# Kernel tuning notes

Measured on AMD Instinct MI355X. Metric: run time of the kernel, lower is better.

## Reference

```python
import jax, jax.numpy as jnp
import numpy as np


def _ln(x, s, b, eps=1e-5):
    m = x.mean(-1, keepdims=True)
    v = ((x - m) ** 2).mean(-1, keepdims=True)
    return (x - m) / jnp.sqrt(v + eps) * s + b


def setup_inputs() -> dict:
    key = jax.random.key(0)
    ks = jax.random.split(key, 12)
    B, T, H, W, C, heads = 4, 4, 16, 16, 128, 8
    N = H * W
    Ntot = T * N
    hid = int(C * 2.66)  # 340

    def rn(k, shape, scale=0.02):
        return jax.random.normal(k, shape, jnp.float32) * scale

    return dict(
        x=jax.random.normal(ks[0], (B, Ntot, C), jnp.float32),
        bias=jax.random.normal(ks[1], (B, Ntot, Ntot), jnp.float32),
        ln1_s=jnp.ones(C), ln1_b=jnp.zeros(C),
        qkv_w=rn(ks[2], (3 * C, C)), qkv_b=jnp.zeros(3 * C),
        proj_w=rn(ks[3], (C, C)), proj_b=jnp.zeros(C),
        bw1=rn(ks[4], (16, 1), 0.5), bb1=jnp.zeros(16),
        bw2=rn(ks[5], (heads, 16), 0.5), bb2=jnp.zeros(heads),
        ln2_s=jnp.ones(C), ln2_b=jnp.zeros(C),
        pin_w=rn(ks[6], (2 * hid, C, 1, 1)), pin_b=jnp.zeros(2 * hid),
        dw_w=rn(ks[7], (2 * hid, 1, 3, 3)), dw_b=jnp.zeros(2 * hid),
        pout_w=rn(ks[8], (C, hid, 1, 1)), pout_b=jnp.zeros(C),
        gamma1=1e-4 * jnp.ones(C), gamma2=1e-4 * jnp.ones(C),
        T=T, H=H, W=W,
    )


def reference(x, bias, ln1_s, ln1_b, qkv_w, qkv_b, proj_w, proj_b,
              bw1, bb1, bw2, bb2, ln2_s, ln2_b,
              pin_w, pin_b, dw_w, dw_b, pout_w, pout_b,
              gamma1, gamma2, T, H, W):
    B, Ntot, C = x.shape
    heads = bw2.shape[0]
    d = C // heads

    # --- attention branch ---
    xn = _ln(x, ln1_s, ln1_b)
    qkv = (xn @ qkv_w.T + qkv_b).reshape(B, Ntot, 3, heads, d).transpose(2, 0, 3, 1, 4)
    q, k, v = qkv[0], qkv[1], qkv[2]  # (B, heads, Ntot, d)
    attn = jnp.einsum('bhnd,bhmd->bhnm', q, k) * (d ** -0.5)
    # NonLinearLieBias: Linear(1,16) -> ReLU -> Linear(16,heads), per (i,j) pair
    lb = jax.nn.relu(bias[..., None] * bw1[:, 0] + bb1) @ bw2.T + bb2  # (B,N,N,heads)
    attn = attn + lb.transpose(0, 3, 1, 2)
    attn = jax.nn.softmax(attn, axis=-1)
    out = jnp.einsum('bhnm,bhmd->bhnd', attn, v).transpose(0, 2, 1, 3).reshape(B, Ntot, C)
    out = out @ proj_w.T + proj_b
    x = x + gamma1 * out

    # --- GDFN branch ---
    N = H * W
    xn2 = _ln(x, ln2_s, ln2_b)
    y = xn2.reshape(B, T, N, C).transpose(0, 1, 3, 2).reshape(B * T, C, H, W)
    dn = ('NCHW', 'OIHW', 'NCHW')
    y = jax.lax.conv_general_dilated(y, pin_w, (1, 1), 'VALID', dimension_numbers=dn) + pin_b[None, :, None, None]
    y = jax.lax.conv_general_dilated(y, dw_w, (1, 1), ((1, 1), (1, 1)), dimension_numbers=dn,
                                     feature_group_count=y.shape[1]) + dw_b[None, :, None, None]
    hid = y.shape[1] // 2
    y = jax.nn.gelu(y[:, :hid], approximate=False) * y[:, hid:]
    y = jax.lax.conv_general_dilated(y, pout_w, (1, 1), 'VALID', dimension_numbers=dn) + pout_b[None, :, None, None]
    y = y.reshape(B, T, C, N).transpose(0, 1, 3, 2).reshape(B, T * N, C)
    x = x + gamma2 * y
    return (x, attn)
```

## Files before the change

kernel.cpp:

```cpp
#include <hip/hip_runtime.h>
#include <hip/hip_bf16.h>
#include <math.h>

#define BB 4
#define NT 1024
#define NSP 256
#define C 128
#define HEADS 8
#define HID 340
#define HID2 680
#define EPS 1e-5f

#define WS_Q    0
#define WS_KT   524288
#define WS_VT   1048576
#define WS_AO   1572864
#define WS_X1   2097152
#define WS_XN2  2621440
#define WS_PIN  3145728
#define WS_GLU  5931008
#define WS_MISC 7323648

typedef __bf16 bf16x8 __attribute__((ext_vector_type(8)));
typedef float f32x4 __attribute__((ext_vector_type(4)));

__global__ void k0_prep(const float* __restrict__ bw1, const float* __restrict__ bb1,
                        const float* __restrict__ bw2, float* __restrict__ misc) {
    int t = threadIdx.x;
    if (t < HEADS) {
        float P = 0.f, Nn = 0.f;
        for (int k = 0; k < 16; ++k) {
            float w1 = bw1[k];
            float w2 = bw2[t * 16 + k];
            if (w1 > 0.f) P += w2 * w1; else Nn += w2 * w1;
        }
        misc[t] = P;
        misc[8 + t] = Nn;
    }
    if (t == 0) {
        int f = 1;
        for (int k = 0; k < 16; ++k) if (bb1[k] != 0.f) f = 0;
        misc[16] = (float)f;
    }
}

__global__ __launch_bounds__(256) void k1_ln_qkv(
    const float* __restrict__ x, const float* __restrict__ s1, const float* __restrict__ b1,
    const float* __restrict__ qkv_w, const float* __restrict__ qkv_b, float* __restrict__ ws) {
    __shared__ float sxn[8][C];
    __shared__ float part[4][2];
    int tid = threadIdx.x;
    int g = tid >> 7, c = tid & 127;
    int wv = tid >> 6, lane = tid & 63;
    int tb = blockIdx.x * 8;

    for (int pass = 0; pass < 4; ++pass) {
        int tok = pass * 2 + g;
        float v = x[(size_t)(tb + tok) * C + c];
        float s = v, sq = v * v;
        #pragma unroll
        for (int off = 32; off; off >>= 1) { s += __shfl_xor(s, off); sq += __shfl_xor(sq, off); }
        if (lane == 0) { part[wv][0] = s; part[wv][1] = sq; }
        __syncthreads();
        float tot = part[g * 2][0] + part[g * 2 + 1][0];
        float tot2 = part[g * 2][1] + part[g * 2 + 1][1];
        float m = tot * (1.0f / C);
        float var = tot2 * (1.0f / C) - m * m;
        float inv = rsqrtf(var + EPS);
        sxn[tok][c] = (v - m) * inv * s1[c] + b1[c];
        __syncthreads();
    }

    float* qw = ws + WS_Q;
    float* ktw = ws + WS_KT;
    float* vtw = ws + WS_VT;
    for (int oo = tid; oo < 384; oo += 256) {
        const float4* wr = (const float4*)(qkv_w + (size_t)oo * C);
        float bbv = qkv_b[oo];
        float acc[8];
        #pragma unroll
        for (int t = 0; t < 8; ++t) acc[t] = bbv;
        #pragma unroll 4
        for (int ic4 = 0; ic4 < 32; ++ic4) {
            float4 w4 = wr[ic4];
            #pragma unroll
            for (int t = 0; t < 8; ++t) {
                acc[t] += w4.x * sxn[t][ic4 * 4 + 0] + w4.y * sxn[t][ic4 * 4 + 1]
                        + w4.z * sxn[t][ic4 * 4 + 2] + w4.w * sxn[t][ic4 * 4 + 3];
            }
        }
        int m3 = oo >> 7, h = (oo >> 4) & 7, dd = oo & 15;
        for (int t = 0; t < 8; ++t) {
            int tok = tb + t;
            int b = tok >> 10, i = tok & 1023;
            if (m3 == 0)      qw[(size_t)tok * C + h * 16 + dd] = acc[t] * 0.25f;
            else if (m3 == 1) ktw[(((size_t)b * 8 + h) * 16 + dd) * NT + i] = acc[t];
            else              vtw[(((size_t)b * 8 + h) * 16 + dd) * NT + i] = acc[t];
        }
    }
}

__global__ __launch_bounds__(256, 4) void k2a_sm(
    const float* __restrict__ bias, const float* __restrict__ bb2v,
    const float* __restrict__ bw1v, const float* __restrict__ bb1v, const float* __restrict__ bw2v,
    const float* __restrict__ ws, float* __restrict__ attn_out) {
    int tid = threadIdx.x;
    int wv = tid >> 6, lane = tid & 63;
    int o = blockIdx.x;
    int blk = (o & 7) * 256 + (o >> 3);
    int b = blk >> 9;
    int quad = (blk >> 1) & 255;
    int hh = blk & 1;
    int i0 = quad << 2;
    int h = hh * 4 + wv;

    const float* misc = ws + WS_MISC;
    float Ph = misc[h], Nh = misc[8 + h], c2 = bb2v[h];
    bool fast = (misc[16] != 0.0f);

    float lg[4][16];
    #pragma unroll
    for (int r = 0; r < 4; ++r) {
        const float* brow = bias + ((size_t)(b * NT + i0 + r)) * NT;
        #pragma unroll
        for (int k = 0; k < 4; ++k) {
            float4 b4 = *(const float4*)(brow + k * 256 + lane * 4);
            float bv[4] = {b4.x, b4.y, b4.z, b4.w};
            #pragma unroll
            for (int cc = 0; cc < 4; ++cc) {
                float bvv = bv[cc];
                float lb;
                if (fast) {
                    lb = bvv * (bvv > 0.f ? Ph : Nh) + c2;
                } else {
                    lb = c2;
                    for (int kk = 0; kk < 16; ++kk) {
                        float t = bvv * bw1v[kk] + bb1v[kk];
                        if (t > 0.f) lb += bw2v[h * 16 + kk] * t;
                    }
                }
                lg[r][k * 4 + cc] = lb;
            }
        }
    }

    const float* ktb = ws + WS_KT + ((size_t)(b * 8 + h) * 16) * NT;
    const float* qb = ws + WS_Q + ((size_t)(b * NT + i0)) * C + h * 16;
    #pragma unroll
    for (int dg = 0; dg < 4; ++dg) {
        float4 q0 = *(const float4*)(qb + 0 * C + dg * 4);
        float4 q1 = *(const float4*)(qb + 1 * C + dg * 4);
        float4 q2 = *(const float4*)(qb + 2 * C + dg * 4);
        float4 q3 = *(const float4*)(qb + 3 * C + dg * 4);
        float qa0[4] = {q0.x, q0.y, q0.z, q0.w};
        float qa1[4] = {q1.x, q1.y, q1.z, q1.w};
        float qa2[4] = {q2.x, q2.y, q2.z, q2.w};
        float qa3[4] = {q3.x, q3.y, q3.z, q3.w};
        #pragma unroll
        for (int dd = 0; dd < 4; ++dd) {
            const float4* kr = (const float4*)(ktb + (size_t)(dg * 4 + dd) * NT);
            #pragma unroll
            for (int k = 0; k < 4; ++k) {
                float4 kv = kr[k * 64 + lane];
                lg[0][k*4+0] += qa0[dd]*kv.x; lg[0][k*4+1] += qa0[dd]*kv.y;
                lg[0][k*4+2] += qa0[dd]*kv.z; lg[0][k*4+3] += qa0[dd]*kv.w;
                lg[1][k*4+0] += qa1[dd]*kv.x; lg[1][k*4+1] += qa1[dd]*kv.y;
                lg[1][k*4+2] += qa1[dd]*kv.z; lg[1][k*4+3] += qa1[dd]*kv.w;
                lg[2][k*4+0] += qa2[dd]*kv.x; lg[2][k*4+1] += qa2[dd]*kv.y;
                lg[2][k*4+2] += qa2[dd]*kv.z; lg[2][k*4+3] += qa2[dd]*kv.w;
                lg[3][k*4+0] += qa3[dd]*kv.x; lg[3][k*4+1] += qa3[dd]*kv.y;
                lg[3][k*4+2] += qa3[dd]*kv.z; lg[3][k*4+3] += qa3[dd]*kv.w;
            }
        }
    }

    #pragma unroll
    for (int r = 0; r < 4; ++r) {
        float mx = lg[r][0];
        #pragma unroll
        for (int k = 1; k < 16; ++k) mx = fmaxf(mx, lg[r][k]);
        #pragma unroll
        for (int off = 32; off; off >>= 1) mx = fmaxf(mx, __shfl_xor(mx, off));
        float s = 0.f;
        #pragma unroll
        for (int k = 0; k < 16; ++k) { lg[r][k] = __expf(lg[r][k] - mx); s += lg[r][k]; }
        #pragma unroll
        for (int off = 32; off; off >>= 1) s += __shfl_xor(s, off);
        float inv = 1.0f / s;
        float* gbase = attn_out + ((size_t)(b * 8 + h) * NT + i0 + r) * NT;
        #pragma unroll
        for (int k = 0; k < 4; ++k) {
            float4 ov;
            ov.x = lg[r][k * 4 + 0] * inv; ov.y = lg[r][k * 4 + 1] * inv;
            ov.z = lg[r][k * 4 + 2] * inv; ov.w = lg[r][k * 4 + 3] * inv;
            *(float4*)(gbase + k * 256 + lane * 4) = ov;
        }
    }
}

__global__ __launch_bounds__(256) void k2b_pv(const float* __restrict__ attn,
                                              const float* __restrict__ ws_ro,
                                              float* __restrict__ ws_out) {
    __shared__ __bf16 sVT[16][1032];
    int tid = threadIdx.x;
    int blk = blockIdx.x;
    int bh = blk >> 4;
    int i0 = (blk & 15) * 64;
    const float* vt = ws_ro + WS_VT + (size_t)bh * 16 * NT;

    #pragma unroll
    for (int s = 0; s < 16; ++s) {
        int f4 = tid + 256 * s;
        int dd = f4 >> 8, jq = f4 & 255;
        float4 v4 = *(const float4*)(vt + ((size_t)dd << 10) + jq * 4);
        sVT[dd][jq * 4 + 0] = (__bf16)v4.x;
        sVT[dd][jq * 4 + 1] = (__bf16)v4.y;
        sVT[dd][jq * 4 + 2] = (__bf16)v4.z;
        sVT[dd][jq * 4 + 3] = (__bf16)v4.w;
    }
    __syncthreads();

    int wv = tid >> 6, lane = tid & 63;
    int row = lane & 15, kg = lane >> 4;
    const float* pbase = attn + ((size_t)bh * NT + i0 + wv * 16 + row) * NT;
    f32x4 acc = {0.f, 0.f, 0.f, 0.f};
    #pragma unroll 4
    for (int kt = 0; kt < 32; ++kt) {
        int k0 = kt * 32 + kg * 8;
        float4 a0 = *(const float4*)(pbase + k0);
        float4 a1 = *(const float4*)(pbase + k0 + 4);
        bf16x8 af;
        af[0] = (__bf16)a0.x; af[1] = (__bf16)a0.y; af[2] = (__bf16)a0.z; af[3] = (__bf16)a0.w;
        af[4] = (__bf16)a1.x; af[5] = (__bf16)a1.y; af[6] = (__bf16)a1.z; af[7] = (__bf16)a1.w;
        bf16x8 bfv = *(const bf16x8*)&sVT[row][k0];
        acc = __builtin_amdgcn_mfma_f32_16x16x32_bf16(af, bfv, acc, 0, 0, 0);
    }
    int b = bh >> 3, h = bh & 7;
    float* ao = ws_out + WS_AO;
    #pragma unroll
    for (int q = 0; q < 4; ++q) {
        int irow = i0 + wv * 16 + kg * 4 + q;
        ao[((size_t)(b * NT + irow)) * C + h * 16 + row] = acc[q];
    }
}

__global__ __launch_bounds__(256) void k3_proj(
    const float* __restrict__ x, const float* __restrict__ proj_w, const float* __restrict__ proj_b,
    const float* __restrict__ g1, const float* __restrict__ s2, const float* __restrict__ b2,
    float* __restrict__ ws) {
    __shared__ float sao[8 * C];
    __shared__ float part[8][4];
    int tid = threadIdx.x;
    int g = tid >> 7, c = tid & 127;
    int wvin = (tid >> 6) & 1, lane = tid & 63;
    int tb = blockIdx.x * 8;
    const float* ao = ws + WS_AO;
    ((float4*)sao)[tid] = ((const float4*)(ao + (size_t)tb * C))[tid];
    __syncthreads();

    float pb = proj_b[c];
    float acc[4] = {pb, pb, pb, pb};
    const float4* wr = (const float4*)(proj_w + (size_t)c * C);
    const float4* a0 = (const float4*)(sao + (g * 4 + 0) * C);
    const float4* a1 = (const float4*)(sao + (g * 4 + 1) * C);
    const float4* a2 = (const float4*)(sao + (g * 4 + 2) * C);
    const float4* a3 = (const float4*)(sao + (g * 4 + 3) * C);
    #pragma unroll 4
    for (int q = 0; q < 32; ++q) {
        float4 w4 = wr[q];
        float4 v0 = a0[q], v1 = a1[q], v2 = a2[q], v3 = a3[q];
        acc[0] += w4.x * v0.x + w4.y * v0.y + w4.z * v0.z + w4.w * v0.w;
        acc[1] += w4.x * v1.x + w4.y * v1.y + w4.z * v1.z + w4.w * v1.w;
        acc[2] += w4.x * v2.x + w4.y * v2.y + w4.z * v2.z + w4.w * v2.w;
        acc[3] += w4.x * v3.x + w4.y * v3.y + w4.z * v3.z + w4.w * v3.w;
    }
    float gv = g1[c], s2v = s2[c], b2v = b2[c];
    float x1v[4];
    #pragma unroll
    for (int t = 0; t < 4; ++t) {
        int tok = tb + g * 4 + t;
        float x1 = x[(size_t)tok * C + c] + gv * acc[t];
        x1v[t] = x1;
        ws[WS_X1 + (size_t)tok * C + c] = x1;
        float s = x1, sq = x1 * x1;
        #pragma unroll
        for (int off = 32; off; off >>= 1) { s += __shfl_xor(s, off); sq += __shfl_xor(sq, off); }
        if (lane == 0) { part[g * 4 + t][wvin * 2] = s; part[g * 4 + t][wvin * 2 + 1] = sq; }
    }
    __syncthreads();
    #pragma unroll
    for (int t = 0; t < 4; ++t) {
        int tok = tb + g * 4 + t;
        float tot = part[g * 4 + t][0] + part[g * 4 + t][2];
        float tot2 = part[g * 4 + t][1] + part[g * 4 + t][3];
        float m = tot * (1.0f / C);
        float var = tot2 * (1.0f / C) - m * m;
        float xn2 = (x1v[t] - m) * rsqrtf(var + EPS) * s2v + b2v;
        int bt = tok >> 8, n = tok & 255;
        ws[WS_XN2 + ((size_t)bt * C + c) * NSP + n] = xn2;
    }
}

__global__ __launch_bounds__(256) void k4_pin(const float* __restrict__ pin_w,
                                              const float* __restrict__ pin_b,
                                              float* __restrict__ ws) {
    __shared__ float sx[C][8];
    int tid = threadIdx.x;
    int bt = blockIdx.x >> 5;
    int n0 = (blockIdx.x & 31) << 3;
    const float* xn2 = ws + WS_XN2;
    float* po = ws + WS_PIN;
    for (int idx = tid; idx < 1024; idx += 256) {
        int ic = idx >> 3, nn = idx & 7;
        sx[ic][nn] = xn2[((size_t)bt * C + ic) * NSP + n0 + nn];
    }
    __syncthreads();
    for (int oc = tid; oc < HID2; oc += 256) {
        const float4* wr = (const float4*)(pin_w + (size_t)oc * C);
        float pb = pin_b[oc];
        float acc[8];
        #pragma unroll
        for (int nn = 0; nn < 8; ++nn) acc[nn] = pb;
        for (int ic4 = 0; ic4 < 32; ++ic4) {
            float4 w4 = wr[ic4];
            #pragma unroll
            for (int nn = 0; nn < 8; ++nn) {
                acc[nn] += w4.x * sx[ic4 * 4 + 0][nn] + w4.y * sx[ic4 * 4 + 1][nn]
                         + w4.z * sx[ic4 * 4 + 2][nn] + w4.w * sx[ic4 * 4 + 3][nn];
            }
        }
        float* ob = po + ((size_t)bt * HID2 + oc) * NSP + n0;
        #pragma unroll
        for (int nn = 0; nn < 8; ++nn) ob[nn] = acc[nn];
    }
}

__global__ __launch_bounds__(256) void k5_dwglu(const float* __restrict__ dw_w,
                                                const float* __restrict__ dw_b,
                                                float* __restrict__ ws) {
    __shared__ float sA[NSP], sG[NSP];
    int bt = blockIdx.x / HID;
    int c = blockIdx.x % HID;
    int px = threadIdx.x;
    int hh = px >> 4, wwp = px & 15;
    const float* po = ws + WS_PIN;
    sA[px] = po[((size_t)bt * HID2 + c) * NSP + px];
    sG[px] = po[((size_t)bt * HID2 + c + HID) * NSP + px];
    __syncthreads();
    float accA = dw_b[c], accG = dw_b[c + HID];
    #pragma unroll
    for (int kh = -1; kh <= 1; ++kh) {
        #pragma unroll
        for (int kw = -1; kw <= 1; ++kw) {
            int h2 = hh + kh, w2 = wwp + kw;
            bool ok = (h2 >= 0) & (h2 < 16) & (w2 >= 0) & (w2 < 16);
            float va = 0.f, vg = 0.f;
            if (ok) { int idx = h2 * 16 + w2; va = sA[idx]; vg = sG[idx]; }
            int kk = (kh + 1) * 3 + (kw + 1);
            accA += va * dw_w[(size_t)c * 9 + kk];
            accG += vg * dw_w[((size_t)c + HID) * 9 + kk];
        }
    }
    float gel = 0.5f * accA * (1.0f + erff(accA * 0.70710678118f));
    ws[WS_GLU + ((size_t)bt * HID + c) * NSP + px] = gel * accG;
}

__global__ __launch_bounds__(128) void k6_pout(const float* __restrict__ pout_w,
                                               const float* __restrict__ pout_b,
                                               const float* __restrict__ g2,
                                               float* __restrict__ ws, float* __restrict__ out) {
    __shared__ float sg[8][HID];
    int tid = threadIdx.x;
    int tb = blockIdx.x * 8;
    int bt = tb >> 8, n0 = tb & 255;
    const float* glu = ws + WS_GLU;
    for (int idx = tid; idx < 8 * HID; idx += 128) {
        int ic = idx >> 3, t = idx & 7;
        sg[t][ic] = glu[((size_t)bt * HID + ic) * NSP + n0 + t];
    }
    __syncthreads();
    int c = tid;
    const float4* wr4 = (const float4*)(pout_w + (size_t)c * HID);
    float acc[8];
    #pragma unroll
    for (int t = 0; t < 8; ++t) acc[t] = 0.f;
    for (int ic4 = 0; ic4 < 85; ++ic4) {
        float4 w4 = wr4[ic4];
        int ic = ic4 * 4;
        #pragma unroll
        for (int t = 0; t < 8; ++t) {
            acc[t] += w4.x * sg[t][ic] + w4.y * sg[t][ic + 1]
                    + w4.z * sg[t][ic + 2] + w4.w * sg[t][ic + 3];
        }
    }
    float pb = pout_b[c], gg = g2[c];
    const float* x1 = ws + WS_X1;
    for (int t = 0; t < 8; ++t) {
        size_t tok = tb + t;
        out[tok * C + c] = x1[tok * C + c] + gg * (acc[t] + pb);
    }
}

extern "C" void kernel_launch(void* const* d_in, const int* in_sizes, int n_in,
                              void* d_out, int out_size, void* d_ws, size_t ws_size,
                              hipStream_t stream) {
    const float* x      = (const float*)d_in[0];
    const float* bias   = (const float*)d_in[1];
    const float* ln1_s  = (const float*)d_in[2];
    const float* ln1_b  = (const float*)d_in[3];
    const float* qkv_w  = (const float*)d_in[4];
    const float* qkv_b  = (const float*)d_in[5];
    const float* proj_w = (const float*)d_in[6];
    const float* proj_b = (const float*)d_in[7];
    const float* bw1    = (const float*)d_in[8];
    const float* bb1    = (const float*)d_in[9];
    const float* bw2    = (const float*)d_in[10];
    const float* bb2    = (const float*)d_in[11];
    const float* ln2_s  = (const float*)d_in[12];
    const float* ln2_b  = (const float*)d_in[13];
    const float* pin_w  = (const float*)d_in[14];
    const float* pin_b  = (const float*)d_in[15];
    const float* dw_w   = (const float*)d_in[16];
    const float* dw_b   = (const float*)d_in[17];
    const float* pout_w = (const float*)d_in[18];
    const float* pout_b = (const float*)d_in[19];
    const float* gamma1 = (const float*)d_in[20];
    const float* gamma2 = (const float*)d_in[21];

    float* ws = (float*)d_ws;
    float* out = (float*)d_out;
    float* attn_out = out + (size_t)BB * NT * C;

    hipLaunchKernelGGL(k0_prep, dim3(1), dim3(64), 0, stream, bw1, bb1, bw2, ws + WS_MISC);
    hipLaunchKernelGGL(k1_ln_qkv, dim3(512), dim3(256), 0, stream, x, ln1_s, ln1_b, qkv_w, qkv_b, ws);
    hipLaunchKernelGGL(k2a_sm, dim3(2048), dim3(256), 0, stream, bias, bb2, bw1, bb1, bw2, ws, attn_out);
    hipLaunchKernelGGL(k2b_pv, dim3(512), dim3(256), 0, stream, attn_out, ws, ws);
    hipLaunchKernelGGL(k3_proj, dim3(512), dim3(256), 0, stream, x, proj_w, proj_b, gamma1, ln2_s, ln2_b, ws);
    hipLaunchKernelGGL(k4_pin, dim3(512), dim3(256), 0, stream, pin_w, pin_b, ws);
    hipLaunchKernelGGL(k5_dwglu, dim3(16 * HID), dim3(256), 0, stream, dw_w, dw_b, ws);
    hipLaunchKernelGGL(k6_pout, dim3(512), dim3(128), 0, stream, pout_w, pout_b, gamma2, ws, out);
}
```

Before: 206.5 us.

## Inline bias-MLP prep into softmax kernel and shrink per-wave rows for occupancy

Drops the separate k0_prep launch, so every wave now computes the folded per-head bias-MLP coefficients from the tiny weight vectors itself. The k2a_sm work mapping changes: each wave handles 2 query rows of one head instead of 4, the grid grows to 4096 blocks, and the launch-bounds occupancy target rises from 4 to 6. The four waves in a block now share one head and cover consecutive row pairs. This is meant to cut register pressure and raise occupancy for the memory-bound bias read and attn write, and to remove one launch. The cost is less K reuse per wave (K is reloaded for every two rows) and redundant coefficient computation in every wave.

Result: no change. 203.9 us (-1.2%).

```diff
diff --git a/kernel.cpp b/kernel.cpp
--- a/kernel.cpp
+++ b/kernel.cpp
@@ -19,30 +19,9 @@
 #define WS_XN2  2621440
 #define WS_PIN  3145728
 #define WS_GLU  5931008
-#define WS_MISC 7323648
 
 typedef __bf16 bf16x8 __attribute__((ext_vector_type(8)));
 typedef float f32x4 __attribute__((ext_vector_type(4)));
-
-__global__ void k0_prep(const float* __restrict__ bw1, const float* __restrict__ bb1,
-                        const float* __restrict__ bw2, float* __restrict__ misc) {
-    int t = threadIdx.x;
-    if (t < HEADS) {
-        float P = 0.f, Nn = 0.f;
-        for (int k = 0; k < 16; ++k) {
-            float w1 = bw1[k];
-            float w2 = bw2[t * 16 + k];
-            if (w1 > 0.f) P += w2 * w1; else Nn += w2 * w1;
-        }
-        misc[t] = P;
-        misc[8 + t] = Nn;
-    }
-    if (t == 0) {
-        int f = 1;
-        for (int k = 0; k < 16; ++k) if (bb1[k] != 0.f) f = 0;
-        misc[16] = (float)f;
-    }
-}
 
 __global__ __launch_bounds__(256) void k1_ln_qkv(
     const float* __restrict__ x, const float* __restrict__ s1, const float* __restrict__ b1,
@@ -100,27 +79,34 @@
     }
 }
 
-__global__ __launch_bounds__(256, 4) void k2a_sm(
+__global__ __launch_bounds__(256, 6) void k2a_sm(
     const float* __restrict__ bias, const float* __restrict__ bb2v,
     const float* __restrict__ bw1v, const float* __restrict__ bb1v, const float* __restrict__ bw2v,
     const float* __restrict__ ws, float* __restrict__ attn_out) {
     int tid = threadIdx.x;
     int wv = tid >> 6, lane = tid & 63;
     int o = blockIdx.x;
-    int blk = (o & 7) * 256 + (o >> 3);
-    int b = blk >> 9;
-    int quad = (blk >> 1) & 255;
-    int hh = blk & 1;
-    int i0 = quad << 2;
-    int h = hh * 4 + wv;
-
-    const float* misc = ws + WS_MISC;
-    float Ph = misc[h], Nh = misc[8 + h], c2 = bb2v[h];
-    bool fast = (misc[16] != 0.0f);
-
-    float lg[4][16];
-    #pragma unroll
-    for (int r = 0; r < 4; ++r) {
+    int blk = (o & 7) * 512 + (o >> 3);
+    int w = blk * 4 + wv;
+    int b = w >> 12;
+    int h = (w >> 9) & 7;
+    int pr = w & 511;
+    int i0 = pr << 1;
+
+    float Ph = 0.f, Nh = 0.f;
+    bool fast = true;
+    #pragma unroll
+    for (int k = 0; k < 16; ++k) {
+        float w1 = bw1v[k];
+        float w2 = bw2v[h * 16 + k];
+        if (w1 > 0.f) Ph += w2 * w1; else Nh += w2 * w1;
+        if (bb1v[k] != 0.f) fast = false;
+    }
+    float c2 = bb2v[h];
+
+    float lg[2][16];
+    #pragma unroll
+    for (int r = 0; r < 2; ++r) {
         const float* brow = bias + ((size_t)(b * NT + i0 + r)) * NT;
         #pragma unroll
         for (int k = 0; k < 4; ++k) {
@@ -150,12 +136,8 @@
     for (int dg = 0; dg < 4; ++dg) {
         float4 q0 = *(const float4*)(qb + 0 * C + dg * 4);
         float4 q1 = *(const float4*)(qb + 1 * C + dg * 4);
-        float4 q2 = *(const float4*)(qb + 2 * C + dg * 4);
-        float4 q3 = *(const float4*)(qb + 3 * C + dg * 4);
         float qa0[4] = {q0.x, q0.y, q0.z, q0.w};
         float qa1[4] = {q1.x, q1.y, q1.z, q1.w};
-        float qa2[4] = {q2.x, q2.y, q2.z, q2.w};
-        float qa3[4] = {q3.x, q3.y, q3.z, q3.w};
         #pragma unroll
         for (int dd = 0; dd < 4; ++dd) {
             const float4* kr = (const float4*)(ktb + (size_t)(dg * 4 + dd) * NT);
@@ -166,16 +148,12 @@
                 lg[0][k*4+2] += qa0[dd]*kv.z; lg[0][k*4+3] += qa0[dd]*kv.w;
                 lg[1][k*4+0] += qa1[dd]*kv.x; lg[1][k*4+1] += qa1[dd]*kv.y;
                 lg[1][k*4+2] += qa1[dd]*kv.z; lg[1][k*4+3] += qa1[dd]*kv.w;
-                lg[2][k*4+0] += qa2[dd]*kv.x; lg[2][k*4+1] += qa2[dd]*kv.y;
-                lg[2][k*4+2] += qa2[dd]*kv.z; lg[2][k*4+3] += qa2[dd]*kv.w;
-                lg[3][k*4+0] += qa3[dd]*kv.x; lg[3][k*4+1] += qa3[dd]*kv.y;
-                lg[3][k*4+2] += qa3[dd]*kv.z; lg[3][k*4+3] += qa3[dd]*kv.w;
             }
         }
     }
 
     #pragma unroll
-    for (int r = 0; r < 4; ++r) {
+    for (int r = 0; r < 2; ++r) {
         float mx = lg[r][0];
         #pragma unroll
         for (int k = 1; k < 16; ++k) mx = fmaxf(mx, lg[r][k]);
@@ -431,9 +409,8 @@
     float* out = (float*)d_out;
     float* attn_out = out + (size_t)BB * NT * C;
 
-    hipLaunchKernelGGL(k0_prep, dim3(1), dim3(64), 0, stream, bw1, bb1, bw2, ws + WS_MISC);
     hipLaunchKernelGGL(k1_ln_qkv, dim3(512), dim3(256), 0, stream, x, ln1_s, ln1_b, qkv_w, qkv_b, ws);
-    hipLaunchKernelGGL(k2a_sm, dim3(2048), dim3(256), 0, stream, bias, bb2, bw1, bb1, bw2, ws, attn_out);
+    hipLaunchKernelGGL(k2a_sm, dim3(4096), dim3(256), 0, stream, bias, bb2, bw1, bb1, bw2, ws, attn_out);
     hipLaunchKernelGGL(k2b_pv, dim3(512), dim3(256), 0, stream, attn_out, ws, ws);
     hipLaunchKernelGGL(k3_proj, dim3(512), dim3(256), 0, stream, x, proj_w, proj_b, gamma1, ln2_s, ln2_b, ws);
     hipLaunchKernelGGL(k4_pin, dim3(512), dim3(256), 0, stream, pin_w, pin_b, ws);
```
